# Kernel optimization log

Measured on AMD Instinct MI355X. Metric: run time of the kernel, lower is better.

Reference implementation:

```python
import jax, jax.numpy as jnp
import numpy as np

# ---- CRF hyperparameters (init_kwargs) ----
NUM_CLASSES = 4
RADIUS = 10            # guided filter radius -> 21x21 kernel
EPS = 1e-4
THETA_GAMMA = 2.5
G_RADIUS = int(THETA_GAMMA * 4)  # gaussian layer radius = 10 -> 21x21 kernel
SPATIAL_COMPAT = 3.0
BILATERAL_COMPAT = 10.0
NUM_ITERATIONS = 5
RGB_W = np.array([0.2989, 0.5870, 0.1140], dtype=np.float32)  # tf rgb_to_grayscale


def _make_kernel(radius, theta):
    x, y = np.mgrid[-radius:radius + 1, -radius:radius + 1]
    k = np.exp(-(x ** 2 + y ** 2) / (2.0 * theta ** 2))
    k = k / k.sum()
    k[radius, radius] = 0.0  # zero out center (no self-message)
    return jnp.asarray(k, dtype=jnp.float32)

_GAUSS_K = _make_kernel(G_RADIUS, THETA_GAMMA)          # spatial gaussian kernel
_GUIDED_K = _make_kernel(RADIUS, RADIUS / 3.0)          # guided-filter gaussian kernel


def _depthwise(src, k2d, r):
    # src: [B,H,W,C], k2d: [kh,kw]; zero-padded depthwise conv (same as pad+VALID)
    c = src.shape[-1]
    kh, kw = k2d.shape
    k = jnp.broadcast_to(k2d[:, :, None, None], (kh, kw, 1, c))
    return jax.lax.conv_general_dilated(
        src, k, window_strides=(1, 1), padding=[(r, r), (r, r)],
        dimension_numbers=('NHWC', 'HWIO', 'NHWC'), feature_group_count=c)


def _gaussian(src):
    return _depthwise(src, _GAUSS_K, G_RADIUS)


def _guided(gray, p):
    # guided gaussian filter with single-channel guide `gray` [B,H,W,1]
    gf = lambda s: _depthwise(s, _GUIDED_K, RADIUS)
    mean_I = gf(gray)                       # [B,H,W,1]
    mean_p = gf(p)                          # [B,H,W,C]
    mean_Ip = gf(gray * p)
    cov_Ip = mean_Ip - mean_I * mean_p
    mean_II = gf(gray * gray)
    var_I = mean_II - mean_I * mean_I
    a = cov_Ip / (var_I + EPS)
    b = mean_p - a * mean_I
    return gf(a) * gray + gf(b)


def setup_inputs() -> dict:
    key = jax.random.key(0)
    k1, k2 = jax.random.split(key)
    unary = jax.random.normal(k1, (1, 512, 512, NUM_CLASSES), dtype=jnp.float32)
    image = jax.random.uniform(k2, (1, 512, 512, 3), dtype=jnp.float32)
    return {"unary": unary, "image": image}


def reference(unary, image):
    gray = (image @ jnp.asarray(RGB_W))[..., None]        # [B,H,W,1]
    ones = jnp.ones_like(unary)
    spatial_norm = _gaussian(ones)
    bilateral_norm = _guided(gray, ones)

    Q = jax.nn.softmax(-unary, axis=-1)
    for _ in range(NUM_ITERATIONS):
        spatial_out = _gaussian(Q) / spatial_norm
        bilateral_out = _guided(gray, Q) / bilateral_norm
        # spatial_weights = SPATIAL_COMPAT*I, bilateral_weights = BILATERAL_COMPAT*I,
        # compatibility = -I  => matmuls reduce to scalar scaling + negation
        message = SPATIAL_COMPAT * spatial_out + BILATERAL_COMPAT * bilateral_out
        pairwise = -message
        Q = jax.nn.softmax(-unary - pairwise, axis=-1)
    return Q
```

## Files before the change

### kernel.cpp

```cpp
#include <hip/hip_runtime.h>
#include <math.h>

#define W 512
#define H 512
#define NPIX (W*H)
#define RAD 10
#define KS 21
#define CRF_EPS 1e-4f

#define TX 32
#define TY 8
#define CIN (TX + 2*RAD)
#define RIN (TY + 2*RAD)
#define GX (W / TX)
#define GY (H / TY)
#define NBLK (GX*GY)
#define NVT (CIN * 4)

struct W21 { float w[KS]; };

__device__ __forceinline__ float4 f4(float x, float y, float z, float w_) {
    return make_float4(x, y, z, w_);
}
__device__ __forceinline__ float4 fma4(float s, float4 a, float4 acc) {
    acc.x = fmaf(s, a.x, acc.x); acc.y = fmaf(s, a.y, acc.y);
    acc.z = fmaf(s, a.z, acc.z); acc.w = fmaf(s, a.w, acc.w);
    return acc;
}
__device__ __forceinline__ int swz(int b, int N) {
    return (b & 7) * (N >> 3) + (b >> 3);
}


__global__ __launch_bounds__(256) void k_init(const float* __restrict__ img,
        const float4* __restrict__ unary, float* __restrict__ gray,
        float4* __restrict__ Q, float* __restrict__ Sg, float* __restrict__ Su,
        W21 wg, W21 wu) {
    int t = threadIdx.x;
    if (blockIdx.x < 2) {
        int x = blockIdx.x * 256 + t;
        float sg = 0.f, su = 0.f;
        #pragma unroll
        for (int d = -RAD; d <= RAD; ++d) {
            int xx = x + d;
            if (xx >= 0 && xx < W) { sg += wg.w[d + RAD]; su += wu.w[d + RAD]; }
        }
        Sg[x] = sg; Su[x] = su;
    }
    int b = swz(blockIdx.x, NPIX / 256);
    int p = b * 256 + t;
    float r = img[3 * p], g = img[3 * p + 1], bch = img[3 * p + 2];
    gray[p] = 0.2989f * r + 0.5870f * g + 0.1140f * bch;
    float4 u = unary[p];
    float mn = fminf(fminf(u.x, u.y), fminf(u.z, u.w));
    float ex = expf(mn - u.x), ey = expf(mn - u.y), ez = expf(mn - u.z), ew = expf(mn - u.w);
    float inv = 1.f / (ex + ey + ez + ew);
    Q[p] = f4(ex * inv, ey * inv, ez * inv, ew * inv);
}

__global__ __launch_bounds__(256, 4) void k_s1(const float* __restrict__ gray,
        const float* __restrict__ Su, float* __restrict__ mean_I,
        float* __restrict__ inv_var, float2* __restrict__ a1b1,
        W21 wu, float c0u) {
    __shared__ float  sg[RIN][CIN];
    __shared__ float2 ii[TY][CIN];
    int L = swz(blockIdx.x, NBLK);
    int x0 = (L & (GX - 1)) * TX, y0 = (L >> 4) * TY;
    int t = threadIdx.x;
    for (int i = t; i < RIN * CIN; i += 256) {
        int r = i / CIN, c = i - r * CIN;
        int gx = x0 + c - RAD, gy = y0 + r - RAD;
        float g = 0.f;
        if ((unsigned)gx < W && (unsigned)gy < H) g = gray[gy * W + gx];
        sg[r][c] = g;
    }
    __syncthreads();
    if (t < NVT) {
        int c = t % CIN, r0 = (t / CIN) * 2;
        float2 acc[2];
        acc[0] = make_float2(0.f, 0.f); acc[1] = acc[0];
        #pragma unroll
        for (int s = 0; s < 22; ++s) {
            float g = sg[r0 + s][c];
            if (s <= 20) { float wg_ = wu.w[s] * g; acc[0].x += wg_; acc[0].y = fmaf(wg_, g, acc[0].y); }
            if (s >= 1)  { float wg_ = wu.w[s-1] * g; acc[1].x += wg_; acc[1].y = fmaf(wg_, g, acc[1].y); }
        }
        ii[r0][c] = acc[0]; ii[r0 + 1][c] = acc[1];
    }
    __syncthreads();
    int row = t >> 5, col = t & 31;
    float2 A = make_float2(0.f, 0.f);
    #pragma unroll
    for (int d = 0; d < KS; ++d) {
        float2 v = ii[row][col + d];
        A.x = fmaf(wu.w[d], v.x, A.x);
        A.y = fmaf(wu.w[d], v.y, A.y);
    }
    int py = y0 + row, px = x0 + col;
    int p = py * W + px;
    float gc = sg[row + RAD][col + RAD];
    float mI = A.x - c0u * gc;
    float mII = A.y - c0u * gc * gc;
    float iv = 1.f / ((mII - mI * mI) + CRF_EPS);
    float N = Su[px] * Su[py] - c0u;
    float av = mI * (1.f - N) * iv;
    float bv = N - av * mI;
    mean_I[p] = mI; inv_var[p] = iv; a1b1[p] = make_float2(av, bv);
}

__global__ __launch_bounds__(256, 4) void k_s2(const float2* __restrict__ a1b1,
        const float* __restrict__ gray, float* __restrict__ inv_bn,
        W21 wu, float c0u) {
    __shared__ float2 s2[RIN][CIN];
    __shared__ float2 ii[TY][CIN];
    int L = swz(blockIdx.x, NBLK);
    int x0 = (L & (GX - 1)) * TX, y0 = (L >> 4) * TY;
    int t = threadIdx.x;
    for (int i = t; i < RIN * CIN; i += 256) {
        int r = i / CIN, c = i - r * CIN;
        int gx = x0 + c - RAD, gy = y0 + r - RAD;
        float2 v = make_float2(0.f, 0.f);
        if ((unsigned)gx < W && (unsigned)gy < H) v = a1b1[gy * W + gx];
        s2[r][c] = v;
    }
    __syncthreads();
    if (t < NVT) {
        int c = t % CIN, r0 = (t / CIN) * 2;
        float2 acc[2];
        acc[0] = make_float2(0.f, 0.f); acc[1] = acc[0];
        #pragma unroll
        for (int s = 0; s < 22; ++s) {
            float2 v = s2[r0 + s][c];
            if (s <= 20) { acc[0].x = fmaf(wu.w[s], v.x, acc[0].x); acc[0].y = fmaf(wu.w[s], v.y, acc[0].y); }
            if (s >= 1)  { acc[1].x = fmaf(wu.w[s-1], v.x, acc[1].x); acc[1].y = fmaf(wu.w[s-1], v.y, acc[1].y); }
        }
        ii[r0][c] = acc[0]; ii[r0 + 1][c] = acc[1];
    }
    __syncthreads();
    int row = t >> 5, col = t & 31;
    float2 A = make_float2(0.f, 0.f);
    #pragma unroll
    for (int d = 0; d < KS; ++d) {
        float2 v = ii[row][col + d];
        A.x = fmaf(wu.w[d], v.x, A.x);
        A.y = fmaf(wu.w[d], v.y, A.y);
    }
    int p = (y0 + row) * W + x0 + col;
    float2 cen = s2[row + RAD][col + RAD];
    float va = A.x - c0u * cen.x;
    float vb = A.y - c0u * cen.y;
    inv_bn[p] = 1.f / (va * gray[p] + vb);
}


__global__ __launch_bounds__(256, 4) void k_f1(const float4* __restrict__ Q,
        const float* __restrict__ gray, const float* __restrict__ mean_I,
        const float* __restrict__ inv_var, const float* __restrict__ Sg,
        const float4* __restrict__ unary, float4* __restrict__ a_out,
        float4* __restrict__ b_out, float4* __restrict__ partial,
        W21 wg, W21 wu, float c0g, float c0u) {
    __shared__ __align__(16) char smem[23296 + 5824 + 6656];
    float4* sQ = (float4*)smem;
    float*  sG = (float*)(smem + 23296);
    float4* i2 = (float4*)(smem + 23296 + 5824);
    float4* i0 = (float4*)smem;
    float4* i1 = (float4*)(smem + 6656);
    int L = swz(blockIdx.x, NBLK);
    int x0 = (L & (GX - 1)) * TX, y0 = (L >> 4) * TY;
    int t = threadIdx.x;
    for (int i = t; i < RIN * CIN; i += 256) {
        int r = i / CIN, c = i - r * CIN;
        int gx = x0 + c - RAD, gy = y0 + r - RAD;
        float4 q = f4(0.f, 0.f, 0.f, 0.f); float g = 0.f;
        if ((unsigned)gx < W && (unsigned)gy < H) {
            int p = gy * W + gx; q = Q[p]; g = gray[p];
        }
        sQ[i] = q; sG[i] = g;
    }
    __syncthreads();
    int row = t >> 5, col = t & 31;
    int py = y0 + row, px = x0 + col;
    int p = py * W + px;
    float mI = mean_I[p], iv = inv_var[p];
    float4 u = unary[p];
    float sgx = Sg[px], sgy = Sg[py];
    float4 Qc = sQ[(row + RAD) * CIN + col + RAD];
    float  gc = sG[(row + RAD) * CIN + col + RAD];
    float4 a0[2], a1[2], a2[2];
    int vc = t % CIN, vr0 = (t / CIN) * 2;
    if (t < NVT) {
        #pragma unroll
        for (int j = 0; j < 2; ++j) { a0[j] = f4(0,0,0,0); a1[j] = a0[j]; a2[j] = a0[j]; }
        #pragma unroll
        for (int s = 0; s < 22; ++s) {
            float4 q = sQ[(vr0 + s) * CIN + vc];
            float g = sG[(vr0 + s) * CIN + vc];
            float4 gq = f4(g * q.x, g * q.y, g * q.z, g * q.w);
            if (s <= 20) {
                a0[0] = fma4(wg.w[s], q, a0[0]);
                a1[0] = fma4(wu.w[s], q, a1[0]);
                a2[0] = fma4(wu.w[s], gq, a2[0]);
            }
            if (s >= 1) {
                a0[1] = fma4(wg.w[s-1], q, a0[1]);
                a1[1] = fma4(wu.w[s-1], q, a1[1]);
                a2[1] = fma4(wu.w[s-1], gq, a2[1]);
            }
        }
    }
    __syncthreads();
    if (t < NVT) {
        #pragma unroll
        for (int j = 0; j < 2; ++j) {
            i0[(vr0 + j) * CIN + vc] = a0[j];
            i1[(vr0 + j) * CIN + vc] = a1[j];
            i2[(vr0 + j) * CIN + vc] = a2[j];
        }
    }
    __syncthreads();
    float4 A0 = f4(0,0,0,0), A1 = A0, A2 = A0;
    #pragma unroll
    for (int d = 0; d < KS; ++d) {
        A0 = fma4(wg.w[d], i0[row * CIN + col + d], A0);
        A1 = fma4(wu.w[d], i1[row * CIN + col + d], A1);
        A2 = fma4(wu.w[d], i2[row * CIN + col + d], A2);
    }
    float4 g4  = fma4(-c0g, Qc, A0);
    float4 m4  = fma4(-c0u, Qc, A1);
    float4 mi4 = fma4(-c0u * gc, Qc, A2);
    float4 a, b;
    a.x = (mi4.x - mI * m4.x) * iv; a.y = (mi4.y - mI * m4.y) * iv;
    a.z = (mi4.z - mI * m4.z) * iv; a.w = (mi4.w - mI * m4.w) * iv;
    b.x = m4.x - a.x * mI; b.y = m4.y - a.y * mI;
    b.z = m4.z - a.z * mI; b.w = m4.w - a.w * mI;
    float s3 = 3.f / (sgx * sgy - c0g);
    float4 part = f4(fmaf(s3, g4.x, -u.x), fmaf(s3, g4.y, -u.y),
                     fmaf(s3, g4.z, -u.z), fmaf(s3, g4.w, -u.w));
    a_out[p] = a; b_out[p] = b; partial[p] = part;
}

__global__ __launch_bounds__(256, 4) void k_f2(const float4* __restrict__ A,
        const float4* __restrict__ B, const float4* __restrict__ partial,
        const float* __restrict__ gray, const float* __restrict__ inv_bn,
        float4* __restrict__ Qout, W21 wu, float c0u) {
    __shared__ __align__(16) char smem[23296 + 6656];
    float4* sT = (float4*)smem;
    float4* ia = (float4*)(smem + 23296);
    float4* ib = (float4*)smem;
    int L = swz(blockIdx.x, NBLK);
    int x0 = (L & (GX - 1)) * TX, y0 = (L >> 4) * TY;
    int t = threadIdx.x;
    int row = t >> 5, col = t & 31;
    int py = y0 + row, px = x0 + col;
    int p = py * W + px;
    int vc = t % CIN, vr0 = (t / CIN) * 2;
    float gv = gray[p];
    float ibn = 10.f * inv_bn[p];
    float4 part = partial[p];
    for (int i = t; i < RIN * CIN; i += 256) {
        int r = i / CIN, c = i - r * CIN;
        int gx = x0 + c - RAD, gy = y0 + r - RAD;
        float4 v = f4(0.f, 0.f, 0.f, 0.f);
        if ((unsigned)gx < W && (unsigned)gy < H) v = A[gy * W + gx];
        sT[i] = v;
    }
    __syncthreads();
    float4 Ac = sT[(row + RAD) * CIN + col + RAD];
    float4 va[2];
    va[0] = f4(0,0,0,0); va[1] = va[0];
    if (t < NVT) {
        #pragma unroll
        for (int s = 0; s < 22; ++s) {
            float4 v = sT[(vr0 + s) * CIN + vc];
            if (s <= 20) va[0] = fma4(wu.w[s], v, va[0]);
            if (s >= 1)  va[1] = fma4(wu.w[s-1], v, va[1]);
        }
        ia[vr0 * CIN + vc] = va[0];
        ia[(vr0 + 1) * CIN + vc] = va[1];
    }
    __syncthreads();
    for (int i = t; i < RIN * CIN; i += 256) {
        int r = i / CIN, c = i - r * CIN;
        int gx = x0 + c - RAD, gy = y0 + r - RAD;
        float4 v = f4(0.f, 0.f, 0.f, 0.f);
        if ((unsigned)gx < W && (unsigned)gy < H) v = B[gy * W + gx];
        sT[i] = v;
    }
    __syncthreads();
    float4 Bc = sT[(row + RAD) * CIN + col + RAD];
    float4 vb[2];
    vb[0] = f4(0,0,0,0); vb[1] = vb[0];
    if (t < NVT) {
        #pragma unroll
        for (int s = 0; s < 22; ++s) {
            float4 v = sT[(vr0 + s) * CIN + vc];
            if (s <= 20) vb[0] = fma4(wu.w[s], v, vb[0]);
            if (s >= 1)  vb[1] = fma4(wu.w[s-1], v, vb[1]);
        }
    }
    __syncthreads();
    if (t < NVT) {
        ib[vr0 * CIN + vc] = vb[0];
        ib[(vr0 + 1) * CIN + vc] = vb[1];
    }
    __syncthreads();
    float4 VA = f4(0,0,0,0), VB = VA;
    #pragma unroll
    for (int d = 0; d < KS; ++d) {
        VA = fma4(wu.w[d], ia[row * CIN + col + d], VA);
        VB = fma4(wu.w[d], ib[row * CIN + col + d], VB);
    }
    float4 a4 = fma4(-c0u, Ac, VA);
    float4 b4 = fma4(-c0u, Bc, VB);
    float lx = fmaf(fmaf(a4.x, gv, b4.x), ibn, part.x);
    float ly = fmaf(fmaf(a4.y, gv, b4.y), ibn, part.y);
    float lz = fmaf(fmaf(a4.z, gv, b4.z), ibn, part.z);
    float lw = fmaf(fmaf(a4.w, gv, b4.w), ibn, part.w);
    float m = fmaxf(fmaxf(lx, ly), fmaxf(lz, lw));
    float ex = expf(lx - m), ey = expf(ly - m), ez = expf(lz - m), ew = expf(lw - m);
    float inv = 1.f / (ex + ey + ez + ew);
    Qout[p] = f4(ex * inv, ey * inv, ez * inv, ew * inv);
}


static void make_w_host(double theta, W21* w, float* c0) {
    double tmp[KS], s = 0.0;
    for (int d = -RAD; d <= RAD; ++d) {
        double v = exp(-(double)(d * d) / (2.0 * theta * theta));
        tmp[d + RAD] = v; s += v;
    }
    for (int i = 0; i < KS; ++i) w->w[i] = (float)(tmp[i] / s);
    *c0 = (float)(1.0 / (s * s));
}

extern "C" void kernel_launch(void* const* d_in, const int* in_sizes, int n_in,
                              void* d_out, int out_size, void* d_ws, size_t ws_size,
                              hipStream_t stream) {
    const float4* unary = (const float4*)d_in[0];
    const float* image = (const float*)d_in[1];
    float* wsf = (float*)d_ws;

    float*  gray    = wsf;
    float*  mean_I  = wsf + 262144;
    float*  inv_var = wsf + 524288;
    float2* a1b1    = (float2*)(wsf + 786432);
    float*  inv_bn  = wsf + 1310720;
    float*  Sg      = wsf + 1572864;
    float*  Su      = wsf + 1573376;
    float4* Q       = (float4*)(wsf + 1573888);
    float4* partial = (float4*)(wsf + 2622464);
    float4* a_arr   = (float4*)(wsf + 3671040);
    float4* b_arr   = (float4*)(wsf + 4719616);

    W21 wg, wu; float c0g, c0u;
    make_w_host(2.5, &wg, &c0g);
    make_w_host(10.0 / 3.0, &wu, &c0u);

    dim3 bl(256), grEl(NPIX / 256), grT(NBLK);

    k_init<<<grEl, bl, 0, stream>>>(image, unary, gray, Q, Sg, Su, wg, wu);
    k_s1<<<grT, bl, 0, stream>>>(gray, Su, mean_I, inv_var, a1b1, wu, c0u);
    k_s2<<<grT, bl, 0, stream>>>(a1b1, gray, inv_bn, wu, c0u);

    for (int it = 0; it < 5; ++it) {
        k_f1<<<grT, bl, 0, stream>>>((const float4*)Q, gray, mean_I, inv_var, Sg,
                                     unary, a_arr, b_arr, partial, wg, wu, c0g, c0u);
        float4* qdst = (it == 4) ? (float4*)d_out : Q;
        k_f2<<<grT, bl, 0, stream>>>(a_arr, b_arr, partial, gray, inv_bn, qdst,
                                     wu, c0u);
    }
}
```

Measured before the change: 173.5 us.

## Fuse all CRF stages into one persistent cooperative kernel with grid syncs

Replaces the chain of thirteen kernel launches with a single cooperative kernel that runs every stage and separates them with grid-wide syncs. Per-pixel values that used to round-trip through global memory (mean_I, inv_var, inv_bn, the partial logits, the normalizer sums) now stay in registers across stages. This removes launch gaps and some global traffic. In exchange it adds grid barrier cost, and the kernel needs every block resident at once (1024 blocks, with launch bounds raised to 5 blocks per CU). If that cannot be met it falls back to the original multi-kernel path.

```diff
diff --git a/kernel.cpp b/kernel.cpp
--- a/kernel.cpp
+++ b/kernel.cpp
@@ -1,5 +1,8 @@
 #include <hip/hip_runtime.h>
+#include <hip/hip_cooperative_groups.h>
 #include <math.h>
+
+namespace cg = cooperative_groups;
 
 #define W 512
 #define H 512
@@ -17,7 +20,23 @@
 #define NBLK (GX*GY)
 #define NVT (CIN * 4)
 
+#define SM_BYTES 29952
+#define OFF_R1 23296
+
 struct W21 { float w[KS]; };
+
+struct Params {
+    const float4* unary;
+    const float*  image;
+    float*  gray;
+    float4* Q;
+    float2* a1b1;
+    float4* a_arr;
+    float4* b_arr;
+    float4* Qfinal;
+    W21 wg, wu;
+    float c0g, c0u;
+};
 
 __device__ __forceinline__ float4 f4(float x, float y, float z, float w_) {
     return make_float4(x, y, z, w_);
@@ -32,7 +51,264 @@
 }
 
 
-__global__ __launch_bounds__(256) void k_init(const float* __restrict__ img,
+__global__ __launch_bounds__(256, 5) void k_crf(Params P) {
+    cg::grid_group grid = cg::this_grid();
+    __shared__ __align__(16) char smem[SM_BYTES];
+    float4* sQ  = (float4*)smem;
+    float2* s2t = (float2*)smem;
+    float2* ii0 = (float2*)smem;
+    float*  sG  = (float*)(smem + OFF_R1);
+    float2* ii1 = (float2*)(smem + OFF_R1);
+    float4* i0  = (float4*)smem;
+    float4* i1  = (float4*)(smem + 6656);
+    float4* i2  = (float4*)(smem + OFF_R1);
+    float4* ia  = (float4*)(smem + OFF_R1);
+    float4* ib  = (float4*)smem;
+
+    int t = threadIdx.x;
+    int L = swz(blockIdx.x, NBLK);
+    int x0 = (L & (GX - 1)) * TX, y0 = (L >> 4) * TY;
+    int row = t >> 5, col = t & 31;
+    int py = y0 + row, px = x0 + col;
+    int p = py * W + px;
+    int vc = t % CIN, vr0 = (t / CIN) * 2;
+    int cidx = (row + RAD) * CIN + col + RAD;
+
+    {
+        int pi = blockIdx.x * 256 + t;
+        float r = P.image[3 * pi], g = P.image[3 * pi + 1], b = P.image[3 * pi + 2];
+        P.gray[pi] = 0.2989f * r + 0.5870f * g + 0.1140f * b;
+        float4 u0 = P.unary[pi];
+        float mn = fminf(fminf(u0.x, u0.y), fminf(u0.z, u0.w));
+        float ex = expf(mn - u0.x), ey = expf(mn - u0.y);
+        float ez = expf(mn - u0.z), ew = expf(mn - u0.w);
+        float inv = 1.f / (ex + ey + ez + ew);
+        P.Q[pi] = f4(ex * inv, ey * inv, ez * inv, ew * inv);
+    }
+    float4 u = P.unary[p];
+    float Sgx = 0.f, Sgy = 0.f, Sux = 0.f, Suy = 0.f;
+    #pragma unroll
+    for (int d = -RAD; d <= RAD; ++d) {
+        int xx = px + d, yy = py + d;
+        if (xx >= 0 && xx < W) { Sgx += P.wg.w[d + RAD]; Sux += P.wu.w[d + RAD]; }
+        if (yy >= 0 && yy < H) { Sgy += P.wg.w[d + RAD]; Suy += P.wu.w[d + RAD]; }
+    }
+    float s3 = 3.f / (Sgx * Sgy - P.c0g);
+    grid.sync();
+
+    for (int i = t; i < RIN * CIN; i += 256) {
+        int r = i / CIN, c = i - r * CIN;
+        int gx = x0 + c - RAD, gy = y0 + r - RAD;
+        float g = 0.f;
+        if ((unsigned)gx < W && (unsigned)gy < H) g = P.gray[gy * W + gx];
+        sG[i] = g;
+    }
+    __syncthreads();
+    if (t < NVT) {
+        float2 acc0 = make_float2(0.f, 0.f), acc1 = acc0;
+        #pragma unroll
+        for (int s = 0; s < 22; ++s) {
+            float g = sG[(vr0 + s) * CIN + vc];
+            if (s <= 20) { float wgv = P.wu.w[s] * g; acc0.x += wgv; acc0.y = fmaf(wgv, g, acc0.y); }
+            if (s >= 1)  { float wgv = P.wu.w[s-1] * g; acc1.x += wgv; acc1.y = fmaf(wgv, g, acc1.y); }
+        }
+        ii0[vr0 * CIN + vc] = acc0;
+        ii0[(vr0 + 1) * CIN + vc] = acc1;
+    }
+    __syncthreads();
+    float gv = sG[cidx];
+    float mI, iv, ibn;
+    {
+        float2 A = make_float2(0.f, 0.f);
+        #pragma unroll
+        for (int d = 0; d < KS; ++d) {
+            float2 v = ii0[row * CIN + col + d];
+            A.x = fmaf(P.wu.w[d], v.x, A.x);
+            A.y = fmaf(P.wu.w[d], v.y, A.y);
+        }
+        mI = A.x - P.c0u * gv;
+        float mII = A.y - P.c0u * gv * gv;
+        iv = 1.f / ((mII - mI * mI) + CRF_EPS);
+        float N = Sux * Suy - P.c0u;
+        float a1v = mI * (1.f - N) * iv;
+        float b1v = N - a1v * mI;
+        P.a1b1[p] = make_float2(a1v, b1v);
+    }
+    grid.sync();
+
+    for (int i = t; i < RIN * CIN; i += 256) {
+        int r = i / CIN, c = i - r * CIN;
+        int gx = x0 + c - RAD, gy = y0 + r - RAD;
+        float2 v = make_float2(0.f, 0.f);
+        if ((unsigned)gx < W && (unsigned)gy < H) v = P.a1b1[gy * W + gx];
+        s2t[i] = v;
+    }
+    __syncthreads();
+    if (t < NVT) {
+        float2 acc0 = make_float2(0.f, 0.f), acc1 = acc0;
+        #pragma unroll
+        for (int s = 0; s < 22; ++s) {
+            float2 v = s2t[(vr0 + s) * CIN + vc];
+            if (s <= 20) { acc0.x = fmaf(P.wu.w[s], v.x, acc0.x); acc0.y = fmaf(P.wu.w[s], v.y, acc0.y); }
+            if (s >= 1)  { acc1.x = fmaf(P.wu.w[s-1], v.x, acc1.x); acc1.y = fmaf(P.wu.w[s-1], v.y, acc1.y); }
+        }
+        ii1[vr0 * CIN + vc] = acc0;
+        ii1[(vr0 + 1) * CIN + vc] = acc1;
+    }
+    __syncthreads();
+    {
+        float2 A = make_float2(0.f, 0.f);
+        #pragma unroll
+        for (int d = 0; d < KS; ++d) {
+            float2 v = ii1[row * CIN + col + d];
+            A.x = fmaf(P.wu.w[d], v.x, A.x);
+            A.y = fmaf(P.wu.w[d], v.y, A.y);
+        }
+        float2 cen = s2t[cidx];
+        float va = A.x - P.c0u * cen.x;
+        float vb = A.y - P.c0u * cen.y;
+        ibn = 10.f / (va * gv + vb);
+    }
+
+    float px_part, py_part, pz_part, pw_part;
+    for (int it = 0; it < 5; ++it) {
+        __syncthreads();
+        for (int i = t; i < RIN * CIN; i += 256) {
+            int r = i / CIN, c = i - r * CIN;
+            int gx = x0 + c - RAD, gy = y0 + r - RAD;
+            float4 q = f4(0.f, 0.f, 0.f, 0.f); float g = 0.f;
+            if ((unsigned)gx < W && (unsigned)gy < H) {
+                int pp = gy * W + gx; q = P.Q[pp]; g = P.gray[pp];
+            }
+            sQ[i] = q; sG[i] = g;
+        }
+        __syncthreads();
+        float4 Qc = sQ[cidx];
+        float4 a0[2], a1r[2], a2[2];
+        if (t < NVT) {
+            #pragma unroll
+            for (int j = 0; j < 2; ++j) { a0[j] = f4(0,0,0,0); a1r[j] = a0[j]; a2[j] = a0[j]; }
+            #pragma unroll
+            for (int s = 0; s < 22; ++s) {
+                float4 q = sQ[(vr0 + s) * CIN + vc];
+                float g = sG[(vr0 + s) * CIN + vc];
+                float4 gq = f4(g * q.x, g * q.y, g * q.z, g * q.w);
+                if (s <= 20) {
+                    a0[0]  = fma4(P.wg.w[s], q, a0[0]);
+                    a1r[0] = fma4(P.wu.w[s], q, a1r[0]);
+                    a2[0]  = fma4(P.wu.w[s], gq, a2[0]);
+                }
+                if (s >= 1) {
+                    a0[1]  = fma4(P.wg.w[s-1], q, a0[1]);
+                    a1r[1] = fma4(P.wu.w[s-1], q, a1r[1]);
+                    a2[1]  = fma4(P.wu.w[s-1], gq, a2[1]);
+                }
+            }
+        }
+        __syncthreads();
+        if (t < NVT) {
+            #pragma unroll
+            for (int j = 0; j < 2; ++j) {
+                i0[(vr0 + j) * CIN + vc] = a0[j];
+                i1[(vr0 + j) * CIN + vc] = a1r[j];
+                i2[(vr0 + j) * CIN + vc] = a2[j];
+            }
+        }
+        __syncthreads();
+        {
+            float4 A0 = f4(0,0,0,0), A1 = A0, A2 = A0;
+            #pragma unroll
+            for (int d = 0; d < KS; ++d) {
+                A0 = fma4(P.wg.w[d], i0[row * CIN + col + d], A0);
+                A1 = fma4(P.wu.w[d], i1[row * CIN + col + d], A1);
+                A2 = fma4(P.wu.w[d], i2[row * CIN + col + d], A2);
+            }
+            float4 g4  = fma4(-P.c0g, Qc, A0);
+            float4 m4  = fma4(-P.c0u, Qc, A1);
+            float4 mi4 = fma4(-P.c0u * gv, Qc, A2);
+            float4 a, b;
+            a.x = (mi4.x - mI * m4.x) * iv; a.y = (mi4.y - mI * m4.y) * iv;
+            a.z = (mi4.z - mI * m4.z) * iv; a.w = (mi4.w - mI * m4.w) * iv;
+            b.x = m4.x - a.x * mI; b.y = m4.y - a.y * mI;
+            b.z = m4.z - a.z * mI; b.w = m4.w - a.w * mI;
+            px_part = fmaf(s3, g4.x, -u.x); py_part = fmaf(s3, g4.y, -u.y);
+            pz_part = fmaf(s3, g4.z, -u.z); pw_part = fmaf(s3, g4.w, -u.w);
+            P.a_arr[p] = a; P.b_arr[p] = b;
+        }
+        grid.sync();
+
+        for (int i = t; i < RIN * CIN; i += 256) {
+            int r = i / CIN, c = i - r * CIN;
+            int gx = x0 + c - RAD, gy = y0 + r - RAD;
+            float4 v = f4(0.f, 0.f, 0.f, 0.f);
+            if ((unsigned)gx < W && (unsigned)gy < H) v = P.a_arr[gy * W + gx];
+            sQ[i] = v;
+        }
+        __syncthreads();
+        float4 Ac = sQ[cidx];
+        if (t < NVT) {
+            float4 va0 = f4(0,0,0,0), va1 = va0;
+            #pragma unroll
+            for (int s = 0; s < 22; ++s) {
+                float4 v = sQ[(vr0 + s) * CIN + vc];
+                if (s <= 20) va0 = fma4(P.wu.w[s], v, va0);
+                if (s >= 1)  va1 = fma4(P.wu.w[s-1], v, va1);
+            }
+            ia[vr0 * CIN + vc] = va0;
+            ia[(vr0 + 1) * CIN + vc] = va1;
+        }
+        __syncthreads();
+        for (int i = t; i < RIN * CIN; i += 256) {
+            int r = i / CIN, c = i - r * CIN;
+            int gx = x0 + c - RAD, gy = y0 + r - RAD;
+            float4 v = f4(0.f, 0.f, 0.f, 0.f);
+            if ((unsigned)gx < W && (unsigned)gy < H) v = P.b_arr[gy * W + gx];
+            sQ[i] = v;
+        }
+        __syncthreads();
+        float4 Bc = sQ[cidx];
+        float4 vb0 = f4(0,0,0,0), vb1 = vb0;
+        if (t < NVT) {
+            #pragma unroll
+            for (int s = 0; s < 22; ++s) {
+                float4 v = sQ[(vr0 + s) * CIN + vc];
+                if (s <= 20) vb0 = fma4(P.wu.w[s], v, vb0);
+                if (s >= 1)  vb1 = fma4(P.wu.w[s-1], v, vb1);
+            }
+        }
+        __syncthreads();
+        if (t < NVT) {
+            ib[vr0 * CIN + vc] = vb0;
+            ib[(vr0 + 1) * CIN + vc] = vb1;
+        }
+        __syncthreads();
+        {
+            float4 VA = f4(0,0,0,0), VB = VA;
+            #pragma unroll
+            for (int d = 0; d < KS; ++d) {
+                VA = fma4(P.wu.w[d], ia[row * CIN + col + d], VA);
+                VB = fma4(P.wu.w[d], ib[row * CIN + col + d], VB);
+            }
+            float4 a4 = fma4(-P.c0u, Ac, VA);
+            float4 b4 = fma4(-P.c0u, Bc, VB);
+            float lx = fmaf(fmaf(a4.x, gv, b4.x), ibn, px_part);
+            float ly = fmaf(fmaf(a4.y, gv, b4.y), ibn, py_part);
+            float lz = fmaf(fmaf(a4.z, gv, b4.z), ibn, pz_part);
+            float lw = fmaf(fmaf(a4.w, gv, b4.w), ibn, pw_part);
+            float m = fmaxf(fmaxf(lx, ly), fmaxf(lz, lw));
+            float ex = expf(lx - m), ey = expf(ly - m);
+            float ez = expf(lz - m), ew = expf(lw - m);
+            float inv = 1.f / (ex + ey + ez + ew);
+            float4 qn = f4(ex * inv, ey * inv, ez * inv, ew * inv);
+            if (it == 4) P.Qfinal[p] = qn;
+            else         P.Q[p] = qn;
+        }
+        if (it < 4) grid.sync();
+    }
+}
+
+
+__global__ __launch_bounds__(256) void fb_init(const float* __restrict__ img,
         const float4* __restrict__ unary, float* __restrict__ gray,
         float4* __restrict__ Q, float* __restrict__ Sg, float* __restrict__ Su,
         W21 wg, W21 wu) {
@@ -58,7 +334,7 @@
     Q[p] = f4(ex * inv, ey * inv, ez * inv, ew * inv);
 }
 
-__global__ __launch_bounds__(256, 4) void k_s1(const float* __restrict__ gray,
+__global__ __launch_bounds__(256, 4) void fb_s1(const float* __restrict__ gray,
         const float* __restrict__ Su, float* __restrict__ mean_I,
         float* __restrict__ inv_var, float2* __restrict__ a1b1,
         W21 wu, float c0u) {
@@ -77,15 +353,14 @@
     __syncthreads();
     if (t < NVT) {
         int c = t % CIN, r0 = (t / CIN) * 2;
-        float2 acc[2];
-        acc[0] = make_float2(0.f, 0.f); acc[1] = acc[0];
+        float2 acc0 = make_float2(0.f, 0.f), acc1 = acc0;
         #pragma unroll
         for (int s = 0; s < 22; ++s) {
             float g = sg[r0 + s][c];
-            if (s <= 20) { float wg_ = wu.w[s] * g; acc[0].x += wg_; acc[0].y = fmaf(wg_, g, acc[0].y); }
-            if (s >= 1)  { float wg_ = wu.w[s-1] * g; acc[1].x += wg_; acc[1].y = fmaf(wg_, g, acc[1].y); }
-        }
-        ii[r0][c] = acc[0]; ii[r0 + 1][c] = acc[1];
+            if (s <= 20) { float wgv = wu.w[s] * g; acc0.x += wgv; acc0.y = fmaf(wgv, g, acc0.y); }
+            if (s >= 1)  { float wgv = wu.w[s-1] * g; acc1.x += wgv; acc1.y = fmaf(wgv, g, acc1.y); }
+        }
+        ii[r0][c] = acc0; ii[r0 + 1][c] = acc1;
     }
     __syncthreads();
     int row = t >> 5, col = t & 31;
@@ -108,7 +383,7 @@
     mean_I[p] = mI; inv_var[p] = iv; a1b1[p] = make_float2(av, bv);
 }
 
-__global__ __launch_bounds__(256, 4) void k_s2(const float2* __restrict__ a1b1,
+__global__ __launch_bounds__(256, 4) void fb_s2(const float2* __restrict__ a1b1,
         const float* __restrict__ gray, float* __restrict__ inv_bn,
         W21 wu, float c0u) {
     __shared__ float2 s2[RIN][CIN];
@@ -126,15 +401,14 @@
     __syncthreads();
     if (t < NVT) {
         int c = t % CIN, r0 = (t / CIN) * 2;
-        float2 acc[2];
-        acc[0] = make_float2(0.f, 0.f); acc[1] = acc[0];
+        float2 acc0 = make_float2(0.f, 0.f), acc1 = acc0;
         #pragma unroll
         for (int s = 0; s < 22; ++s) {
             float2 v = s2[r0 + s][c];
-            if (s <= 20) { acc[0].x = fmaf(wu.w[s], v.x, acc[0].x); acc[0].y = fmaf(wu.w[s], v.y, acc[0].y); }
-            if (s >= 1)  { acc[1].x = fmaf(wu.w[s-1], v.x, acc[1].x); acc[1].y = fmaf(wu.w[s-1], v.y, acc[1].y); }
-        }
-        ii[r0][c] = acc[0]; ii[r0 + 1][c] = acc[1];
+            if (s <= 20) { acc0.x = fmaf(wu.w[s], v.x, acc0.x); acc0.y = fmaf(wu.w[s], v.y, acc0.y); }
+            if (s >= 1)  { acc1.x = fmaf(wu.w[s-1], v.x, acc1.x); acc1.y = fmaf(wu.w[s-1], v.y, acc1.y); }
+        }
+        ii[r0][c] = acc0; ii[r0 + 1][c] = acc1;
     }
     __syncthreads();
     int row = t >> 5, col = t & 31;
@@ -152,8 +426,7 @@
     inv_bn[p] = 1.f / (va * gray[p] + vb);
 }
 
-
-__global__ __launch_bounds__(256, 4) void k_f1(const float4* __restrict__ Q,
+__global__ __launch_bounds__(256, 4) void fb_f1(const float4* __restrict__ Q,
         const float* __restrict__ gray, const float* __restrict__ mean_I,
         const float* __restrict__ inv_var, const float* __restrict__ Sg,
         const float4* __restrict__ unary, float4* __restrict__ a_out,
@@ -239,7 +512,7 @@
     a_out[p] = a; b_out[p] = b; partial[p] = part;
 }
 
-__global__ __launch_bounds__(256, 4) void k_f2(const float4* __restrict__ A,
+__global__ __launch_bounds__(256, 4) void fb_f2(const float4* __restrict__ A,
         const float4* __restrict__ B, const float4* __restrict__ partial,
         const float* __restrict__ gray, const float* __restrict__ inv_bn,
         float4* __restrict__ Qout, W21 wu, float c0u) {
@@ -266,17 +539,16 @@
     }
     __syncthreads();
     float4 Ac = sT[(row + RAD) * CIN + col + RAD];
-    float4 va[2];
-    va[0] = f4(0,0,0,0); va[1] = va[0];
+    float4 va0 = f4(0,0,0,0), va1 = va0;
     if (t < NVT) {
         #pragma unroll
         for (int s = 0; s < 22; ++s) {
             float4 v = sT[(vr0 + s) * CIN + vc];
-            if (s <= 20) va[0] = fma4(wu.w[s], v, va[0]);
-            if (s >= 1)  va[1] = fma4(wu.w[s-1], v, va[1]);
-        }
-        ia[vr0 * CIN + vc] = va[0];
-        ia[(vr0 + 1) * CIN + vc] = va[1];
+            if (s <= 20) va0 = fma4(wu.w[s], v, va0);
+            if (s >= 1)  va1 = fma4(wu.w[s-1], v, va1);
+        }
+        ia[vr0 * CIN + vc] = va0;
+        ia[(vr0 + 1) * CIN + vc] = va1;
     }
     __syncthreads();
     for (int i = t; i < RIN * CIN; i += 256) {
@@ -288,20 +560,19 @@
     }
     __syncthreads();
     float4 Bc = sT[(row + RAD) * CIN + col + RAD];
-    float4 vb[2];
-    vb[0] = f4(0,0,0,0); vb[1] = vb[0];
+    float4 vb0 = f4(0,0,0,0), vb1 = vb0;
     if (t < NVT) {
         #pragma unroll
         for (int s = 0; s < 22; ++s) {
             float4 v = sT[(vr0 + s) * CIN + vc];
-            if (s <= 20) vb[0] = fma4(wu.w[s], v, vb[0]);
-            if (s >= 1)  vb[1] = fma4(wu.w[s-1], v, vb[1]);
-        }
-    }
-    __syncthreads();
-    if (t < NVT) {
-        ib[vr0 * CIN + vc] = vb[0];
-        ib[(vr0 + 1) * CIN + vc] = vb[1];
+            if (s <= 20) vb0 = fma4(wu.w[s], v, vb0);
+            if (s >= 1)  vb1 = fma4(wu.w[s-1], v, vb1);
+        }
+    }
+    __syncthreads();
+    if (t < NVT) {
+        ib[vr0 * CIN + vc] = vb0;
+        ib[(vr0 + 1) * CIN + vc] = vb1;
     }
     __syncthreads();
     float4 VA = f4(0,0,0,0), VB = VA;
@@ -356,17 +627,37 @@
     make_w_host(2.5, &wg, &c0g);
     make_w_host(10.0 / 3.0, &wu, &c0u);
 
-    dim3 bl(256), grEl(NPIX / 256), grT(NBLK);
-
-    k_init<<<grEl, bl, 0, stream>>>(image, unary, gray, Q, Sg, Su, wg, wu);
-    k_s1<<<grT, bl, 0, stream>>>(gray, Su, mean_I, inv_var, a1b1, wu, c0u);
-    k_s2<<<grT, bl, 0, stream>>>(a1b1, gray, inv_bn, wu, c0u);
-
-    for (int it = 0; it < 5; ++it) {
-        k_f1<<<grT, bl, 0, stream>>>((const float4*)Q, gray, mean_I, inv_var, Sg,
-                                     unary, a_arr, b_arr, partial, wg, wu, c0g, c0u);
-        float4* qdst = (it == 4) ? (float4*)d_out : Q;
-        k_f2<<<grT, bl, 0, stream>>>(a_arr, b_arr, partial, gray, inv_bn, qdst,
-                                     wu, c0u);
-    }
-}
+    int dev = 0;
+    (void)hipGetDevice(&dev);
+    int coop = 0, nCU = 0, blkPerCU = 0;
+    (void)hipDeviceGetAttribute(&coop, hipDeviceAttributeCooperativeLaunch, dev);
+    (void)hipDeviceGetAttribute(&nCU, hipDeviceAttributeMultiprocessorCount, dev);
+    (void)hipOccupancyMaxActiveBlocksPerMultiprocessor(&blkPerCU,
+            (const void*)k_crf, 256, 0);
+    bool useCoop = (coop != 0) && ((long)blkPerCU * nCU >= NBLK);
+
+    hipError_t st = hipErrorUnknown;
+    if (useCoop) {
+        Params P;
+        P.unary = unary; P.image = image; P.gray = gray; P.Q = Q;
+        P.a1b1 = a1b1; P.a_arr = a_arr; P.b_arr = b_arr;
+        P.Qfinal = (float4*)d_out;
+        P.wg = wg; P.wu = wu; P.c0g = c0g; P.c0u = c0u;
+        void* args[] = { &P };
+        st = hipLaunchCooperativeKernel((const void*)k_crf, dim3(NBLK), dim3(256),
+                                        args, 0, stream);
+    }
+    if (st != hipSuccess) {
+        dim3 bl(256), grEl(NPIX / 256), grT(NBLK);
+        fb_init<<<grEl, bl, 0, stream>>>(image, unary, gray, Q, Sg, Su, wg, wu);
+        fb_s1<<<grT, bl, 0, stream>>>(gray, Su, mean_I, inv_var, a1b1, wu, c0u);
+        fb_s2<<<grT, bl, 0, stream>>>(a1b1, gray, inv_bn, wu, c0u);
+        for (int it = 0; it < 5; ++it) {
+            fb_f1<<<grT, bl, 0, stream>>>(Q, gray, mean_I, inv_var, Sg,
+                                          unary, a_arr, b_arr, partial, wg, wu, c0g, c0u);
+            float4* qdst = (it == 4) ? (float4*)d_out : Q;
+            fb_f2<<<grT, bl, 0, stream>>>(a_arr, b_arr, partial, gray, inv_bn, qdst,
+                                          wu, c0u);
+        }
+    }
+}
```

Measured after the change: 170.5 us. Within noise of the previous version (-1.7%).
